# Kernel optimization log

Hardware: AMD Instinct MI355X
Metric: run time of the kernel (lower is better)

Reference implementation:

```python
import jax, jax.numpy as jnp
import numpy as np

KERNEL_SIZE = 5
GROUP_SIZE = 1
SCALE = 2


def setup_inputs() -> dict:
    key = jax.random.key(0)
    k1, k2 = jax.random.split(key)
    features = jax.random.normal(k1, (8, 256, 64, 64), dtype=jnp.float32)
    masks = jax.random.uniform(k2, (8, KERNEL_SIZE * KERNEL_SIZE * GROUP_SIZE, 64 * SCALE, 64 * SCALE), dtype=jnp.float32)
    return {"features": features, "masks": masks}


def _carafe_naive(features, masks, k, g, s):
    n, c, h, w = features.shape
    cg = c // g
    pad = (k - 1) // 2
    fp = jnp.pad(features, ((0, 0), (0, 0), (pad, pad), (pad, pad)))
    # im2col patches, matching F.unfold ordering: channel outer, kernel
    # positions row-major inner -> [n, c, k*k, h, w]
    patches = jnp.stack(
        [fp[:, :, i:i + h, j:j + w] for i in range(k) for j in range(k)],
        axis=2,
    )
    feat = patches.reshape(n, g, cg, k * k, h, w)          # n g c i h w
    ker = masks.reshape(n, g, k * k, h, s, w, s)           # n g i h a w b
    # per-pixel dynamic conv over the k*k window, fused with upsample
    out = jnp.einsum('ngcihw,ngihawb->ngchawb', feat, ker)  # n g c h a w b
    return out.reshape(n, c, h * s, w * s)


def reference(features, masks):
    return _carafe_naive(features, masks, KERNEL_SIZE, GROUP_SIZE, SCALE)
```

## Files before the change

### kernel.cpp

```cpp
#include <hip/hip_runtime.h>

#define K 5
#define N_ 8
#define C_ 256
#define H_ 64
#define W_ 64
#define HW (H_ * W_)
#define HO 128
#define WO 128
#define HOWO (HO * WO)
#define HB 4
#define CCHUNK 32
#define UC 4
#define NGROUP (CCHUNK / UC)
#define LDS_R (HB + K - 1)
#define LDS_C 68
#define POS (LDS_R * LDS_C)

typedef __attribute__((ext_vector_type(2))) float f2;

__global__ __launch_bounds__(256)
void carafe_row_kernel(const float* __restrict__ feat,
                       const float* __restrict__ mask,
                       float* __restrict__ out) {
    const int ht = blockIdx.x;
    const int zc = blockIdx.y;
    const int n  = zc >> 3;
    const int c0 = (zc & 7) * CCHUNK;
    const int h0 = ht * HB;

    const int tid = threadIdx.x;
    const int r   = tid >> 6;
    const int c   = tid & 63;
    const int hb  = h0 + r;

    f2 m0[K * K], m1[K * K];
    {
        const f2* mb = (const f2*)(mask + (size_t)n * (K * K) * HOWO
                                        + (size_t)(2 * hb) * WO + 2 * c);
        #pragma unroll
        for (int i = 0; i < K * K; ++i) {
            m0[i] = mb[(size_t)i * (HOWO / 2)];
            m1[i] = mb[(size_t)i * (HOWO / 2) + WO / 2];
        }
    }

    int off[3]; bool val[3];
    #pragma unroll
    for (int i = 0; i < 3; ++i) {
        int p  = tid + i * 256;
        int rr = p / LDS_C, cc = p - rr * LDS_C;
        int hs = h0 - 2 + rr;
        int ws = cc - 2;
        val[i] = (p < POS) && (hs >= 0) && (hs < H_) && (ws >= 0) && (ws < W_);
        off[i] = hs * W_ + ws;
    }

    __shared__ float4 lds[2][POS];

    const float* fbase = feat + (size_t)n * C_ * HW;
    float*       obase = out  + (size_t)n * C_ * HOWO
                              + (size_t)(2 * hb) * WO + 2 * c;

    float sreg[3][UC];
    auto stage_load = [&](int cbase) {
        const float* fp = fbase + (size_t)cbase * HW;
        #pragma unroll
        for (int i = 0; i < 3; ++i)
            #pragma unroll
            for (int u = 0; u < UC; ++u)
                sreg[i][u] = val[i] ? fp[u * HW + off[i]] : 0.f;
    };
    auto stage_write = [&](int buf) {
        #pragma unroll
        for (int i = 0; i < 3; ++i) {
            int p = tid + i * 256;
            if (p < POS)
                lds[buf][p] = make_float4(sreg[i][0], sreg[i][1],
                                          sreg[i][2], sreg[i][3]);
        }
    };

    stage_load(c0);
    stage_write(0);
    __syncthreads();

    const int rbase = r * LDS_C + c;

    for (int g = 0; g < NGROUP; ++g) {
        const int buf = g & 1;

        if (g + 1 < NGROUP) stage_load(c0 + (g + 1) * UC);

        const float4* Ls = &lds[buf][rbase];
        f2 a0[4], a1[4];
        #pragma unroll
        for (int u = 0; u < 4; ++u) { a0[u] = (f2)0.f; a1[u] = (f2)0.f; }
        #pragma unroll
        for (int ki = 0; ki < K; ++ki) {
            #pragma unroll
            for (int kj = 0; kj < K; ++kj) {
                float4 f  = Ls[ki * LDS_C + kj];
                f2 w0m = m0[ki * K + kj];
                f2 w1m = m1[ki * K + kj];
                a0[0] += f.x * w0m;  a1[0] += f.x * w1m;
                a0[1] += f.y * w0m;  a1[1] += f.y * w1m;
                a0[2] += f.z * w0m;  a1[2] += f.z * w1m;
                a0[3] += f.w * w0m;  a1[3] += f.w * w1m;
            }
        }
        #pragma unroll
        for (int u = 0; u < 4; ++u) {
            f2* op = (f2*)(obase + (size_t)(c0 + g * UC + u) * HOWO);
            __builtin_nontemporal_store(a0[u], op);
            __builtin_nontemporal_store(a1[u], op + WO / 2);
        }

        if (g + 1 < NGROUP) {
            stage_write(buf ^ 1);
            __syncthreads();
        }
    }
}

extern "C" void kernel_launch(void* const* d_in, const int* in_sizes, int n_in,
                              void* d_out, int out_size, void* d_ws, size_t ws_size,
                              hipStream_t stream) {
    const float* feat = (const float*)d_in[0];
    const float* mask = (const float*)d_in[1];
    float* out = (float*)d_out;

    dim3 grid(H_ / HB, N_ * (C_ / CCHUNK));
    dim3 block(256);
    carafe_row_kernel<<<grid, block, 0, stream>>>(feat, mask, out);
}
```

Before: 45.65 us.

## Replace LDS-staged tile with direct per-thread global loads of 5x5 windows

Removes the shared-memory tile, its barriers and the double buffering. Each thread now loads its 25-tap window straight from global memory using clamped offsets, and padding is handled by zeroing the mask weights for out-of-range taps. It processes one channel at a time and software-pipelines across two register buffers. This drops LDS traffic and synchronisation but issues 25 scalar global loads per channel per thread and relies on L1/L2 to absorb the heavy overlap between neighbouring threads' windows.

```diff
diff --git a/kernel.cpp b/kernel.cpp
--- a/kernel.cpp
+++ b/kernel.cpp
@@ -1,6 +1,7 @@
 #include <hip/hip_runtime.h>
 
 #define K 5
+#define KK (K * K)
 #define N_ 8
 #define C_ 256
 #define H_ 64
@@ -11,18 +12,13 @@
 #define HOWO (HO * WO)
 #define HB 4
 #define CCHUNK 32
-#define UC 4
-#define NGROUP (CCHUNK / UC)
-#define LDS_R (HB + K - 1)
-#define LDS_C 68
-#define POS (LDS_R * LDS_C)
 
 typedef __attribute__((ext_vector_type(2))) float f2;
 
 __global__ __launch_bounds__(256)
-void carafe_row_kernel(const float* __restrict__ feat,
-                       const float* __restrict__ mask,
-                       float* __restrict__ out) {
+void carafe_direct_kernel(const float* __restrict__ feat,
+                          const float* __restrict__ mask,
+                          float* __restrict__ out) {
     const int ht = blockIdx.x;
     const int zc = blockIdx.y;
     const int n  = zc >> 3;
@@ -34,92 +30,66 @@
     const int c   = tid & 63;
     const int hb  = h0 + r;
 
-    f2 m0[K * K], m1[K * K];
+    f2 m0[KK], m1[KK];
     {
-        const f2* mb = (const f2*)(mask + (size_t)n * (K * K) * HOWO
+        const f2* mb = (const f2*)(mask + (size_t)n * KK * HOWO
                                         + (size_t)(2 * hb) * WO + 2 * c);
         #pragma unroll
-        for (int i = 0; i < K * K; ++i) {
+        for (int i = 0; i < KK; ++i) {
             m0[i] = mb[(size_t)i * (HOWO / 2)];
             m1[i] = mb[(size_t)i * (HOWO / 2) + WO / 2];
         }
+        #pragma unroll
+        for (int ki = 0; ki < K; ++ki) {
+            bool vr = (hb - 2 + ki >= 0) && (hb - 2 + ki < H_);
+            #pragma unroll
+            for (int kj = 0; kj < K; ++kj) {
+                bool vc = (c - 2 + kj >= 0) && (c - 2 + kj < W_);
+                if (!(vr && vc)) { m0[ki * K + kj] = (f2)0.f; m1[ki * K + kj] = (f2)0.f; }
+            }
+        }
     }
 
-    int off[3]; bool val[3];
+    int off[KK];
     #pragma unroll
-    for (int i = 0; i < 3; ++i) {
-        int p  = tid + i * 256;
-        int rr = p / LDS_C, cc = p - rr * LDS_C;
-        int hs = h0 - 2 + rr;
-        int ws = cc - 2;
-        val[i] = (p < POS) && (hs >= 0) && (hs < H_) && (ws >= 0) && (ws < W_);
-        off[i] = hs * W_ + ws;
+    for (int ki = 0; ki < K; ++ki) {
+        int hs = hb - 2 + ki; hs = hs < 0 ? 0 : (hs > H_ - 1 ? H_ - 1 : hs);
+        #pragma unroll
+        for (int kj = 0; kj < K; ++kj) {
+            int ws = c - 2 + kj; ws = ws < 0 ? 0 : (ws > W_ - 1 ? W_ - 1 : ws);
+            off[ki * K + kj] = hs * W_ + ws;
+        }
     }
-
-    __shared__ float4 lds[2][POS];
 
     const float* fbase = feat + (size_t)n * C_ * HW;
     float*       obase = out  + (size_t)n * C_ * HOWO
                               + (size_t)(2 * hb) * WO + 2 * c;
 
-    float sreg[3][UC];
-    auto stage_load = [&](int cbase) {
-        const float* fp = fbase + (size_t)cbase * HW;
+    auto load_ch = [&](float* v, int cc) {
+        const float* fp = fbase + (size_t)cc * HW;
         #pragma unroll
-        for (int i = 0; i < 3; ++i)
-            #pragma unroll
-            for (int u = 0; u < UC; ++u)
-                sreg[i][u] = val[i] ? fp[u * HW + off[i]] : 0.f;
+        for (int i = 0; i < KK; ++i) v[i] = fp[off[i]];
     };
-    auto stage_write = [&](int buf) {
+    auto compute_store = [&](const float* v, int cc) {
+        f2 a0 = (f2)0.f, a1 = (f2)0.f;
         #pragma unroll
-        for (int i = 0; i < 3; ++i) {
-            int p = tid + i * 256;
-            if (p < POS)
-                lds[buf][p] = make_float4(sreg[i][0], sreg[i][1],
-                                          sreg[i][2], sreg[i][3]);
+        for (int i = 0; i < KK; ++i) {
+            a0 += v[i] * m0[i];
+            a1 += v[i] * m1[i];
         }
+        f2* op = (f2*)(obase + (size_t)cc * HOWO);
+        __builtin_nontemporal_store(a0, op);
+        __builtin_nontemporal_store(a1, op + WO / 2);
     };
 
-    stage_load(c0);
-    stage_write(0);
-    __syncthreads();
-
-    const int rbase = r * LDS_C + c;
-
-    for (int g = 0; g < NGROUP; ++g) {
-        const int buf = g & 1;
-
-        if (g + 1 < NGROUP) stage_load(c0 + (g + 1) * UC);
-
-        const float4* Ls = &lds[buf][rbase];
-        f2 a0[4], a1[4];
-        #pragma unroll
-        for (int u = 0; u < 4; ++u) { a0[u] = (f2)0.f; a1[u] = (f2)0.f; }
-        #pragma unroll
-        for (int ki = 0; ki < K; ++ki) {
-            #pragma unroll
-            for (int kj = 0; kj < K; ++kj) {
-                float4 f  = Ls[ki * LDS_C + kj];
-                f2 w0m = m0[ki * K + kj];
-                f2 w1m = m1[ki * K + kj];
-                a0[0] += f.x * w0m;  a1[0] += f.x * w1m;
-                a0[1] += f.y * w0m;  a1[1] += f.y * w1m;
-                a0[2] += f.z * w0m;  a1[2] += f.z * w1m;
-                a0[3] += f.w * w0m;  a1[3] += f.w * w1m;
-            }
-        }
-        #pragma unroll
-        for (int u = 0; u < 4; ++u) {
-            f2* op = (f2*)(obase + (size_t)(c0 + g * UC + u) * HOWO);
-            __builtin_nontemporal_store(a0[u], op);
-            __builtin_nontemporal_store(a1[u], op + WO / 2);
-        }
-
-        if (g + 1 < NGROUP) {
-            stage_write(buf ^ 1);
-            __syncthreads();
-        }
+    float va[KK], vb[KK];
+    load_ch(va, c0);
+    #pragma unroll 1
+    for (int cc = c0; cc < c0 + CCHUNK; cc += 2) {
+        load_ch(vb, cc + 1);
+        compute_store(va, cc);
+        if (cc + 2 < c0 + CCHUNK) load_ch(va, cc + 2);
+        compute_store(vb, cc + 1);
     }
 }
 
@@ -132,5 +102,5 @@
 
     dim3 grid(H_ / HB, N_ * (C_ / CCHUNK));
     dim3 block(256);
-    carafe_row_kernel<<<grid, block, 0, stream>>>(feat, mask, out);
+    carafe_direct_kernel<<<grid, block, 0, stream>>>(feat, mask, out);
 }
```

Result: slower. 84.29 us (+84.7%).
